# Performance work log

Hardware: AMD Instinct MI355X
Metric: run time of the kernel (lower is better)

## Reference

```python
import jax, jax.numpy as jnp
import numpy as np

V = 25  # number of skeleton joints (hard-coded in the original module)

def setup_inputs() -> dict:
    key = jax.random.key(0)
    k1, k2 = jax.random.split(key)
    shape = (256, 3, 600, 25, 2)  # N, C, T, V, M
    x = jax.random.normal(k1, shape, dtype=jnp.float32)
    y = jax.random.normal(k2, shape, dtype=jnp.float32)
    return {"x": x, "y": y}

def reference(x, y):
    # x, y: (N, C, T, V, M)
    # temporal motion: difference along T
    motion = x[:, :, 1:, :, :] - x[:, :, :-1, :, :]            # (N, C, T-1, V, M)
    # per-(sample, joint) mean absolute motion over C, T-1, M
    mean_move = jnp.mean(jnp.abs(motion), axis=(1, 2, 4))      # (N, V)
    # normalize per sample so ratios sum to V (=25)
    ratio = V * mean_move / jnp.sum(mean_move, axis=1, keepdims=True)  # (N, V)
    # weighted squared error, mean over all elements
    sq = (x - y) ** 2                                          # (N, C, T, V, M)
    weighted = sq * ratio[:, None, None, :, None]
    return jnp.mean(weighted)
```

## Files before the change

kernel.cpp:

```cpp
#include <hip/hip_runtime.h>

#define N_ 256
#define C_ 3
#define T_ 600
#define V_ 25
#define M_ 2
#define NSLAB (N_ * C_)
#define TY 20
#define CH (T_ / TY)

__global__ __launch_bounds__(512) void slab_kernel(const float* __restrict__ x,
                                                   const float* __restrict__ y,
                                                   float* __restrict__ absP,
                                                   float* __restrict__ sqP) {
    const int slab = blockIdx.x;
    const int tx   = threadIdx.x;
    const int ty   = threadIdx.y;

    const float2* __restrict__ xs = reinterpret_cast<const float2*>(x) + (size_t)slab * (T_ * V_);
    const float2* __restrict__ ys = reinterpret_cast<const float2*>(y) + (size_t)slab * (T_ * V_);

    const int t0 = ty * CH;
    const int t1 = t0 + CH;

    float2 xc = xs[t0 * V_ + tx];
    float2 yc = ys[t0 * V_ + tx];
    float ex = xc.x - yc.x, ey = xc.y - yc.y;
    float sq = ex * ex + ey * ey;
    float mv = 0.0f;

    for (int t = t0 + 1; t < t1; ++t) {
        float2 xn = xs[t * V_ + tx];
        float2 yn = ys[t * V_ + tx];
        mv += fabsf(xn.x - xc.x) + fabsf(xn.y - xc.y);
        ex = xn.x - yn.x; ey = xn.y - yn.y;
        sq += ex * ex + ey * ey;
        xc = xn;
    }
    if (t1 < T_) {
        float2 xn = xs[t1 * V_ + tx];
        mv += fabsf(xn.x - xc.x) + fabsf(xn.y - xc.y);
    }

    __shared__ float redA[TY][V_ + 1];
    __shared__ float redS[TY][V_ + 1];
    redA[ty][tx] = mv;
    redS[ty][tx] = sq;
    __syncthreads();

    if (ty == 0) {
        float a = 0.0f, s = 0.0f;
        #pragma unroll
        for (int j = 0; j < TY; ++j) { a += redA[j][tx]; s += redS[j][tx]; }
        absP[slab * V_ + tx] = a;
        sqP[slab * V_ + tx]  = s;
    }
}

__global__ __launch_bounds__(256) void finalize_kernel(const float* __restrict__ absP,
                                                       const float* __restrict__ sqP,
                                                       float* __restrict__ out) {
    const int n = threadIdx.x;
    float av[V_], sv[V_];
    #pragma unroll
    for (int v = 0; v < V_; ++v) { av[v] = 0.0f; sv[v] = 0.0f; }
    #pragma unroll
    for (int c = 0; c < C_; ++c) {
        const int base = (n * C_ + c) * V_;
        #pragma unroll
        for (int v = 0; v < V_; ++v) {
            av[v] += absP[base + v];
            sv[v] += sqP[base + v];
        }
    }
    float sumAbs = 0.0f, sumW = 0.0f;
    #pragma unroll
    for (int v = 0; v < V_; ++v) { sumAbs += av[v]; sumW += av[v] * sv[v]; }
    float partial = (float)V_ * sumW / sumAbs;

    __shared__ float red[256];
    red[n] = partial;
    __syncthreads();
    for (int s = 128; s > 0; s >>= 1) {
        if (n < s) red[n] += red[n + s];
        __syncthreads();
    }
    if (n == 0) out[0] = red[0] / (float)((size_t)N_ * C_ * T_ * V_ * M_);
}

extern "C" void kernel_launch(void* const* d_in, const int* in_sizes, int n_in,
                              void* d_out, int out_size, void* d_ws, size_t ws_size,
                              hipStream_t stream) {
    const float* x = (const float*)d_in[0];
    const float* y = (const float*)d_in[1];
    float* out  = (float*)d_out;
    float* absP = (float*)d_ws;
    float* sqP  = absP + NSLAB * V_;

    dim3 blk(V_, TY);
    slab_kernel<<<NSLAB, blk, 0, stream>>>(x, y, absP, sqP);

    finalize_kernel<<<1, 256, 0, stream>>>(absP, sqP, out);
}
```

Measured before the change: 40.19 us.

## Fuse finalize into slab kernel using atomic counters and last-block reduction

Merges the separate finalize kernel into the main slab kernel. Per-slab partials are published with atomics, a per-sample counter picks the last of the C slabs to compute that sample's weighted contribution, and a global counter picks the final block to write the output. This removes a second kernel launch and its serialized single-block reduction, but adds a hipMemsetAsync on the workspace before each launch plus atomic traffic and memory-ordering work.

```diff
diff --git a/kernel.cpp b/kernel.cpp
--- a/kernel.cpp
+++ b/kernel.cpp
@@ -9,13 +9,16 @@
 #define TY 20
 #define CH (T_ / TY)
 
-__global__ __launch_bounds__(512) void slab_kernel(const float* __restrict__ x,
-                                                   const float* __restrict__ y,
-                                                   float* __restrict__ absP,
-                                                   float* __restrict__ sqP) {
+__global__ __launch_bounds__(512) void fused_kernel(
+    const float* __restrict__ x, const float* __restrict__ y,
+    float* __restrict__ absP, float* __restrict__ sqP,
+    float* __restrict__ accOut, int* __restrict__ cntN, int* __restrict__ cntAll,
+    float* __restrict__ out)
+{
     const int slab = blockIdx.x;
     const int tx   = threadIdx.x;
     const int ty   = threadIdx.y;
+    const int n    = slab / C_;
 
     const float2* __restrict__ xs = reinterpret_cast<const float2*>(x) + (size_t)slab * (T_ * V_);
     const float2* __restrict__ ys = reinterpret_cast<const float2*>(y) + (size_t)slab * (T_ * V_);
@@ -44,48 +47,53 @@
 
     __shared__ float redA[TY][V_ + 1];
     __shared__ float redS[TY][V_ + 1];
+    __shared__ int lastFlag;
     redA[ty][tx] = mv;
     redS[ty][tx] = sq;
     __syncthreads();
 
+    float a = 0.0f, s = 0.0f;
     if (ty == 0) {
-        float a = 0.0f, s = 0.0f;
         #pragma unroll
         for (int j = 0; j < TY; ++j) { a += redA[j][tx]; s += redS[j][tx]; }
-        absP[slab * V_ + tx] = a;
-        sqP[slab * V_ + tx]  = s;
-    }
-}
-
-__global__ __launch_bounds__(256) void finalize_kernel(const float* __restrict__ absP,
-                                                       const float* __restrict__ sqP,
-                                                       float* __restrict__ out) {
-    const int n = threadIdx.x;
-    float av[V_], sv[V_];
-    #pragma unroll
-    for (int v = 0; v < V_; ++v) { av[v] = 0.0f; sv[v] = 0.0f; }
-    #pragma unroll
-    for (int c = 0; c < C_; ++c) {
-        const int base = (n * C_ + c) * V_;
-        #pragma unroll
-        for (int v = 0; v < V_; ++v) {
-            av[v] += absP[base + v];
-            sv[v] += sqP[base + v];
+        atomicAdd(&absP[slab * V_ + tx], a);
+        atomicAdd(&sqP [slab * V_ + tx], s);
+        if (tx == 0) {
+            int old = __hip_atomic_fetch_add(&cntN[n], 1, __ATOMIC_ACQ_REL, __HIP_MEMORY_SCOPE_AGENT);
+            lastFlag = (old == C_ - 1) ? 1 : 0;
         }
     }
-    float sumAbs = 0.0f, sumW = 0.0f;
-    #pragma unroll
-    for (int v = 0; v < V_; ++v) { sumAbs += av[v]; sumW += av[v] * sv[v]; }
-    float partial = (float)V_ * sumW / sumAbs;
+    __syncthreads();
 
-    __shared__ float red[256];
-    red[n] = partial;
-    __syncthreads();
-    for (int s = 128; s > 0; s >>= 1) {
-        if (n < s) red[n] += red[n + s];
+    if (lastFlag) {
+        __shared__ float sA[V_], sW[V_];
+        if (ty == 0) {
+            const int myc = slab - n * C_;
+            float aN = a, sN = s;
+            #pragma unroll
+            for (int c = 0; c < C_; ++c) {
+                if (c == myc) continue;
+                const int idx = (n * C_ + c) * V_ + tx;
+                aN += atomicAdd(&absP[idx], 0.0f);
+                sN += atomicAdd(&sqP [idx], 0.0f);
+            }
+            sA[tx] = aN;
+            sW[tx] = aN * sN;
+        }
         __syncthreads();
+        if (ty == 0 && tx == 0) {
+            float sumA = 0.0f, sumW = 0.0f;
+            #pragma unroll
+            for (int v = 0; v < V_; ++v) { sumA += sA[v]; sumW += sW[v]; }
+            const float contrib = (float)V_ * sumW / sumA;
+            atomicAdd(accOut, contrib);
+            const int done = __hip_atomic_fetch_add(cntAll, 1, __ATOMIC_ACQ_REL, __HIP_MEMORY_SCOPE_AGENT);
+            if (done == N_ - 1) {
+                const float tot = atomicAdd(accOut, 0.0f);
+                out[0] = tot / 23040000.0f;
+            }
+        }
     }
-    if (n == 0) out[0] = red[0] / (float)((size_t)N_ * C_ * T_ * V_ * M_);
 }
 
 extern "C" void kernel_launch(void* const* d_in, const int* in_sizes, int n_in,
@@ -93,12 +101,17 @@
                               hipStream_t stream) {
     const float* x = (const float*)d_in[0];
     const float* y = (const float*)d_in[1];
-    float* out  = (float*)d_out;
-    float* absP = (float*)d_ws;
-    float* sqP  = absP + NSLAB * V_;
+    float* out    = (float*)d_out;
+
+    float* absP   = (float*)d_ws;
+    float* sqP    = absP + NSLAB * V_;
+    float* accOut = sqP + NSLAB * V_;
+    int*   cntN   = (int*)(accOut + 1);
+    int*   cntAll = cntN + N_;
+
+    const size_t zbytes = (size_t)(2 * NSLAB * V_ + 1 + N_ + 1) * 4;
+    hipMemsetAsync(d_ws, 0, zbytes, stream);
 
     dim3 blk(V_, TY);
-    slab_kernel<<<NSLAB, blk, 0, stream>>>(x, y, absP, sqP);
-
-    finalize_kernel<<<1, 256, 0, stream>>>(absP, sqP, out);
+    fused_kernel<<<NSLAB, blk, 0, stream>>>(x, y, absP, sqP, accOut, cntN, cntAll, out);
 }
```

Measured after the change: 72.88 us. 81.3% more time.
